# Kernel optimization log

Hardware: AMD Instinct MI355X
Metric: run time of the kernel (lower is better)

The kernel has to match this reference:

```python
import jax, jax.numpy as jnp
import numpy as np

B, L, H = 4096, 512, 32  # batch, latent_dim, hidden_size


def setup_inputs() -> dict:
    key = jax.random.key(0)
    ks = jax.random.split(key, 8)
    mu = jax.random.normal(ks[0], (B, L), jnp.float32)
    log_var = jax.random.normal(ks[1], (B, L), jnp.float32)
    eps0 = jax.random.normal(ks[2], (B,), jnp.float32)
    eps = jax.random.normal(ks[3], (B, L), jnp.float32)
    # Per-step MiniSampler params. Sampler idx has in_size = idx+1.
    # Zero-pad first-layer weights to [L, H, L]; row idx only uses cols 0..idx.
    mask = (jnp.arange(L)[None, :] <= jnp.arange(L)[:, None]).astype(jnp.float32)  # [L, L]
    W1 = jax.random.normal(ks[4], (L, H, L), jnp.float32) * 0.1 * mask[:, None, :]
    b1 = jax.random.normal(ks[5], (L, H), jnp.float32) * 0.1
    W2 = jax.random.normal(ks[6], (L, 2, H), jnp.float32) * 0.1
    b2 = jax.random.normal(ks[7], (L, 2), jnp.float32) * 0.1
    return {"mu": mu, "log_var": log_var, "eps0": eps0, "eps": eps,
            "W1": W1, "b1": b1, "W2": W2, "b2": b2}


def reference(mu, log_var, eps0, eps, W1, b1, W2, b2):
    # sample=False path (the default). First latent is reparameterized:
    std0 = jnp.exp(0.5 * log_var[:, 0])
    input0 = eps0 * std0 + mu[:, 0]                      # [B]
    # Input to sampler idx is [input0, mu[:,0], ..., mu[:,idx-1]];
    # W1 is column-masked so one shared padded vector works for all steps.
    v = jnp.concatenate([input0[:, None], mu[:, :-1]], axis=1)  # [B, L]
    h = jax.nn.leaky_relu(jnp.einsum('bj,ihj->bih', v, W1) + b1[None])  # [B, L, H]
    out = jnp.einsum('bih,ioh->bio', h, W2) + b2[None]   # [B, L, 2]
    mus_resampled = out[..., 0]                          # [B, L]
    log_vars_resampled = out[..., 1]                     # [B, L]
    samples = eps * jnp.exp(0.5 * log_vars_resampled) + mus_resampled  # [B, L]
    return (mus_resampled, log_vars_resampled, samples)
```

## Files before the change

### kernel.cpp

```cpp
#include <hip/hip_runtime.h>
#include <hip/hip_bf16.h>

#define Bn 4096
#define Ln 512
#define Hn 32
#define MT 4

using bf16x8 = __attribute__((ext_vector_type(8))) __bf16;
using f32x4  = __attribute__((ext_vector_type(4))) float;

#define GLOAD_LDS16(g, l)                                                          \
  __builtin_amdgcn_global_load_lds(                                                \
      (const __attribute__((address_space(1))) void*)(g),                          \
      (__attribute__((address_space(3))) void*)(l), 16, 0, 0)

__device__ __forceinline__ unsigned short f2bf(float x) {
  unsigned int u = __float_as_uint(x);
  unsigned int r = (u + 0x7FFFu + ((u >> 16) & 1u)) >> 16;
  return (unsigned short)r;
}

__global__ __launch_bounds__(256) void prep_w1_kernel(const float* __restrict__ W1,
                                                      unsigned short* __restrict__ W1b) {
  int idx = blockIdx.x * 256 + threadIdx.x;
  const float4 f = reinterpret_cast<const float4*>(W1)[idx];
  ushort4 o;
  o.x = f2bf(f.x); o.y = f2bf(f.y); o.z = f2bf(f.z); o.w = f2bf(f.w);
  reinterpret_cast<ushort4*>(W1b)[idx] = o;
}

__global__ __launch_bounds__(256) void prep_v_kernel(const float* __restrict__ mu,
                                                     const float* __restrict__ log_var,
                                                     const float* __restrict__ eps0,
                                                     unsigned short* __restrict__ Vb) {
  int idx = blockIdx.x * 256 + threadIdx.x;
  int b = idx >> 9, j = idx & 511;
  float v;
  if (j == 0) {
    v = eps0[b] * expf(0.5f * log_var[(size_t)b * Ln]) + mu[(size_t)b * Ln];
  } else {
    v = mu[(size_t)b * Ln + j - 1];
  }
  Vb[idx] = f2bf(v);
}

__global__ __launch_bounds__(256) void gemm_fused_kernel(
    const unsigned short* __restrict__ Vb,
    const unsigned short* __restrict__ W1b,
    const float* __restrict__ b1,
    const float* __restrict__ W2,
    const float* __restrict__ b2,
    const float* __restrict__ eps,
    float* __restrict__ out)
{
  const int tid  = threadIdx.x;
  const int wid  = tid >> 6;
  const int lane = tid & 63;
  const int l15  = lane & 15;
  const int lq   = lane >> 4;

  const int bid = blockIdx.x;
  const int bn  = 127 - (bid >> 3);
  const int mg  = bid & 7;
  const int mb  = mg * (MT * 128);
  const int nb  = bn * 128;

  const int ksteps = min(8, (bn + 16) >> 4);

  __shared__ unsigned short As[2 * 128 * 64];
  __shared__ unsigned short Bs[2 * 128 * 64];

  const int rowc = lane >> 3;
  const int sswz = (lane & 7) ^ rowc;
  const unsigned short* gA = Vb  + (size_t)(mb + wid * 32 + rowc) * Ln + sswz * 8;
  const unsigned short* gB = W1b + (size_t)(nb + wid * 32 + rowc) * Ln + sswz * 8;
  unsigned short* lA = As + wid * 2048;
  unsigned short* lB = Bs + wid * 2048;

  auto STAGE = [&](int buf, int mt, int k0e) {
    const int    lofs = buf * 8192;
    const size_t ga   = (size_t)mt * (128 * Ln) + k0e;
#pragma unroll
    for (int j = 0; j < 4; ++j) {
      GLOAD_LDS16(gA + ga + (size_t)j * 8 * Ln, lA + lofs + j * 512);
      GLOAD_LDS16(gB + k0e + (size_t)j * 8 * Ln, lB + lofs + j * 512);
    }
  };

  const int arow = (wid >> 1) * 64 + l15;
  const int brow = (wid & 1) * 64 + l15;
  const int swz7 = l15 & 7;

  f32x4 acc[4][4];
#pragma unroll
  for (int fn = 0; fn < 4; ++fn)
#pragma unroll
    for (int fm = 0; fm < 4; ++fm) acc[fn][fm] = f32x4{0.f, 0.f, 0.f, 0.f};

  auto COMPUTE = [&](int buf) {
    const int cofs = buf * 8192;
#pragma unroll
    for (int ks2 = 0; ks2 < 2; ++ks2) {
      const int se = ((ks2 * 4 + lq) ^ swz7) * 8;
      bf16x8 a[4], b[4];
#pragma unroll
      for (int f = 0; f < 4; ++f) {
        a[f] = *reinterpret_cast<const bf16x8*>(As + cofs + (arow + f * 16) * 64 + se);
        b[f] = *reinterpret_cast<const bf16x8*>(Bs + cofs + (brow + f * 16) * 64 + se);
      }
#pragma unroll
      for (int fn = 0; fn < 4; ++fn)
#pragma unroll
        for (int fm = 0; fm < 4; ++fm)
          acc[fn][fm] = __builtin_amdgcn_mfma_f32_16x16x32_bf16(b[fn], a[fm], acc[fn][fm], 0, 0, 0);
    }
  };

  float* mus = out;
  float* lvs = out + (size_t)Bn * Ln;
  float* smp = out + (size_t)2 * Bn * Ln;

  int buf = 0;
  STAGE(0, 0, 0);

  for (int mt = 0; mt < MT; ++mt) {
    for (int k = 0; k < ksteps; ++k) {
      int kn = k + 1, mtn = mt;
      if (kn == ksteps) { kn = 0; ++mtn; }
      if (mtn < MT) {
        STAGE(buf ^ 1, mtn, kn * 64);
        asm volatile("s_waitcnt vmcnt(8)" ::: "memory");
      } else {
        asm volatile("s_waitcnt vmcnt(0)" ::: "memory");
      }
      __builtin_amdgcn_s_barrier();
      __builtin_amdgcn_sched_barrier(0);
      COMPUTE(buf);

      if (k == ksteps - 1) {
        float* S = reinterpret_cast<float*>(Bs + buf * 8192);
        __builtin_amdgcn_s_barrier();

        const int wrow = (wid >> 1) * 64;
#pragma unroll
        for (int il = 0; il < 2; ++il) {
          const int i   = bn * 4 + (wid & 1) * 2 + il;
          const int icl = (wid & 1) * 2 + il;
          float4 b1q[2], w20q[2], w21q[2];
#pragma unroll
          for (int q = 0; q < 2; ++q) {
            const int hb = q * 16 + lq * 4;
            b1q[q]  = *reinterpret_cast<const float4*>(b1 + i * Hn + hb);
            w20q[q] = *reinterpret_cast<const float4*>(W2 + (i * 2 + 0) * Hn + hb);
            w21q[q] = *reinterpret_cast<const float4*>(W2 + (i * 2 + 1) * Hn + hb);
          }
          const float bias0 = b2[i * 2 + 0];
          const float bias1 = b2[i * 2 + 1];
#pragma unroll
          for (int fm = 0; fm < 4; ++fm) {
            float p0 = 0.f, p1 = 0.f;
#pragma unroll
            for (int q = 0; q < 2; ++q) {
              const f32x4& A = acc[il * 2 + q][fm];
              const float* b1f = reinterpret_cast<const float*>(&b1q[q]);
              const float* w0f = reinterpret_cast<const float*>(&w20q[q]);
              const float* w1f = reinterpret_cast<const float*>(&w21q[q]);
#pragma unroll
              for (int r = 0; r < 4; ++r) {
                float x  = A[r] + b1f[r];
                float hv = (x >= 0.f) ? x : 0.01f * x;
                p0 += hv * w0f[r];
                p1 += hv * w1f[r];
              }
            }
            p0 += __shfl_xor(p0, 16);
            p0 += __shfl_xor(p0, 32);
            p1 += __shfl_xor(p1, 16);
            p1 += __shfl_xor(p1, 32);
            if (lq == 0) {
              const int r = wrow + fm * 16 + l15;
              S[icl * 128 + r]       = p0 + bias0;
              S[512 + icl * 128 + r] = p1 + bias1;
            }
          }
        }
        asm volatile("s_waitcnt lgkmcnt(0)" ::: "memory");
        __builtin_amdgcn_s_barrier();

        if (tid < 128) {
          const int    r = tid;
          const size_t o = (size_t)(mb + mt * 128 + r) * Ln + bn * 4;
          float4 muv, lvv;
          muv.x = S[r];       muv.y = S[128 + r]; muv.z = S[256 + r]; muv.w = S[384 + r];
          lvv.x = S[512 + r]; lvv.y = S[640 + r]; lvv.z = S[768 + r]; lvv.w = S[896 + r];
          const float4 ep = *reinterpret_cast<const float4*>(eps + o);
          float4 sm;
          sm.x = ep.x * expf(0.5f * lvv.x) + muv.x;
          sm.y = ep.y * expf(0.5f * lvv.y) + muv.y;
          sm.z = ep.z * expf(0.5f * lvv.z) + muv.z;
          sm.w = ep.w * expf(0.5f * lvv.w) + muv.w;
          *reinterpret_cast<float4*>(mus + o) = muv;
          *reinterpret_cast<float4*>(lvs + o) = lvv;
          *reinterpret_cast<float4*>(smp + o) = sm;
        }
#pragma unroll
        for (int fn = 0; fn < 4; ++fn)
#pragma unroll
          for (int fm = 0; fm < 4; ++fm) acc[fn][fm] = f32x4{0.f, 0.f, 0.f, 0.f};
      }
      __builtin_amdgcn_s_barrier();
      buf ^= 1;
    }
  }
}

extern "C" void kernel_launch(void* const* d_in, const int* in_sizes, int n_in,
                              void* d_out, int out_size, void* d_ws, size_t ws_size,
                              hipStream_t stream) {
  const float* mu      = (const float*)d_in[0];
  const float* log_var = (const float*)d_in[1];
  const float* eps0    = (const float*)d_in[2];
  const float* eps     = (const float*)d_in[3];
  const float* W1      = (const float*)d_in[4];
  const float* b1      = (const float*)d_in[5];
  const float* W2      = (const float*)d_in[6];
  const float* b2      = (const float*)d_in[7];
  float* out = (float*)d_out;

  unsigned short* Vb  = (unsigned short*)d_ws;
  unsigned short* W1b = (unsigned short*)((char*)d_ws + (size_t)Bn * Ln * 2);

  prep_v_kernel<<<(Bn * Ln) / 256, 256, 0, stream>>>(mu, log_var, eps0, Vb);
  prep_w1_kernel<<<(Ln * Hn * Ln) / 4 / 256, 256, 0, stream>>>(W1, W1b);
  gemm_fused_kernel<<<128 * (32 / MT), 256, 0, stream>>>(
      Vb, W1b, b1, W2, b2, eps, out);
}
```

Measured before the change: 85.64 us.

## Load A operands directly to registers, skip masked W1 reads, remap blocks per XCD

The GEMM kernel no longer stages the V (A) tile through LDS. Each wave loads its A fragments straight from global memory into registers before the barrier, which halves LDS usage and allows an occupancy hint of 3 blocks per CU. Blocks are remapped so each XCD gets a balanced mix of triangular column tiles. The W1 conversion kernel skips reading the zero-masked upper triangle and writes zeros instead, and leaky_relu and exp are replaced with fmax and exp2. The risks are uncoalesced direct global loads of A and the changed vmcnt accounting.

Result: slower. 127.1 us (+48.4%).

```diff
diff --git a/kernel.cpp b/kernel.cpp
--- a/kernel.cpp
+++ b/kernel.cpp
@@ -23,9 +23,16 @@
 __global__ __launch_bounds__(256) void prep_w1_kernel(const float* __restrict__ W1,
                                                       unsigned short* __restrict__ W1b) {
   int idx = blockIdx.x * 256 + threadIdx.x;
-  const float4 f = reinterpret_cast<const float4*>(W1)[idx];
+  const int n  = idx >> 7;
+  const int c0 = (idx & 127) * 4;
+  const int i  = n >> 5;
   ushort4 o;
-  o.x = f2bf(f.x); o.y = f2bf(f.y); o.z = f2bf(f.z); o.w = f2bf(f.w);
+  if (c0 > i) {
+    o.x = 0; o.y = 0; o.z = 0; o.w = 0;
+  } else {
+    const float4 f = reinterpret_cast<const float4*>(W1)[idx];
+    o.x = f2bf(f.x); o.y = f2bf(f.y); o.z = f2bf(f.z); o.w = f2bf(f.w);
+  }
   reinterpret_cast<ushort4*>(W1b)[idx] = o;
 }
 
@@ -44,7 +51,7 @@
   Vb[idx] = f2bf(v);
 }
 
-__global__ __launch_bounds__(256) void gemm_fused_kernel(
+__global__ __launch_bounds__(256, 3) void gemm_fused_kernel(
     const unsigned short* __restrict__ Vb,
     const unsigned short* __restrict__ W1b,
     const float* __restrict__ b1,
@@ -59,35 +66,32 @@
   const int l15  = lane & 15;
   const int lq   = lane >> 4;
 
-  const int bid = blockIdx.x;
-  const int bn  = 127 - (bid >> 3);
-  const int mg  = bid & 7;
-  const int mb  = mg * (MT * 128);
-  const int nb  = bn * 128;
+  const int bid  = blockIdx.x;
+  const int xcd  = bid & 7;
+  const int s    = bid >> 3;
+  const int g    = xcd + 8 * (3 - (s >> 5));
+  const int bn   = g * 4 + ((s >> 3) & 3);
+  const int mg   = s & 7;
+  const int mb   = mg * (MT * 128);
+  const int nb   = bn * 128;
 
   const int ksteps = min(8, (bn + 16) >> 4);
 
-  __shared__ unsigned short As[2 * 128 * 64];
   __shared__ unsigned short Bs[2 * 128 * 64];
 
   const int rowc = lane >> 3;
   const int sswz = (lane & 7) ^ rowc;
-  const unsigned short* gA = Vb  + (size_t)(mb + wid * 32 + rowc) * Ln + sswz * 8;
   const unsigned short* gB = W1b + (size_t)(nb + wid * 32 + rowc) * Ln + sswz * 8;
-  unsigned short* lA = As + wid * 2048;
   unsigned short* lB = Bs + wid * 2048;
 
-  auto STAGE = [&](int buf, int mt, int k0e) {
-    const int    lofs = buf * 8192;
-    const size_t ga   = (size_t)mt * (128 * Ln) + k0e;
-#pragma unroll
-    for (int j = 0; j < 4; ++j) {
-      GLOAD_LDS16(gA + ga + (size_t)j * 8 * Ln, lA + lofs + j * 512);
-      GLOAD_LDS16(gB + k0e + (size_t)j * 8 * Ln, lB + lofs + j * 512);
-    }
+  auto STAGE_B = [&](int buf, int k0e) {
+#pragma unroll
+    for (int j = 0; j < 4; ++j)
+      GLOAD_LDS16(gB + k0e + (size_t)j * 8 * Ln, lB + buf * 8192 + j * 512);
   };
 
-  const int arow = (wid >> 1) * 64 + l15;
+  const unsigned short* gA = Vb + (size_t)(mb + (wid >> 1) * 64 + l15) * Ln;
+
   const int brow = (wid & 1) * 64 + l15;
   const int swz7 = l15 & 7;
 
@@ -96,46 +100,55 @@
   for (int fn = 0; fn < 4; ++fn)
 #pragma unroll
     for (int fm = 0; fm < 4; ++fm) acc[fn][fm] = f32x4{0.f, 0.f, 0.f, 0.f};
-
-  auto COMPUTE = [&](int buf) {
-    const int cofs = buf * 8192;
-#pragma unroll
-    for (int ks2 = 0; ks2 < 2; ++ks2) {
-      const int se = ((ks2 * 4 + lq) ^ swz7) * 8;
-      bf16x8 a[4], b[4];
-#pragma unroll
-      for (int f = 0; f < 4; ++f) {
-        a[f] = *reinterpret_cast<const bf16x8*>(As + cofs + (arow + f * 16) * 64 + se);
-        b[f] = *reinterpret_cast<const bf16x8*>(Bs + cofs + (brow + f * 16) * 64 + se);
-      }
-#pragma unroll
-      for (int fn = 0; fn < 4; ++fn)
-#pragma unroll
-        for (int fm = 0; fm < 4; ++fm)
-          acc[fn][fm] = __builtin_amdgcn_mfma_f32_16x16x32_bf16(b[fn], a[fm], acc[fn][fm], 0, 0, 0);
-    }
-  };
 
   float* mus = out;
   float* lvs = out + (size_t)Bn * Ln;
   float* smp = out + (size_t)2 * Bn * Ln;
 
   int buf = 0;
-  STAGE(0, 0, 0);
+  STAGE_B(0, 0);
 
   for (int mt = 0; mt < MT; ++mt) {
     for (int k = 0; k < ksteps; ++k) {
       int kn = k + 1, mtn = mt;
       if (kn == ksteps) { kn = 0; ++mtn; }
-      if (mtn < MT) {
-        STAGE(buf ^ 1, mtn, kn * 64);
+      const bool more = (mtn < MT);
+      if (more) STAGE_B(buf ^ 1, kn * 64);
+
+      bf16x8 a[2][4];
+      {
+        const unsigned short* pa = gA + (size_t)mt * (128 * Ln) + k * 64;
+#pragma unroll
+        for (int ks2 = 0; ks2 < 2; ++ks2)
+#pragma unroll
+          for (int f = 0; f < 4; ++f)
+            a[ks2][f] = *reinterpret_cast<const bf16x8*>(
+                pa + (size_t)f * 16 * Ln + (ks2 * 4 + lq) * 8);
+      }
+
+      if (more) {
+        asm volatile("s_waitcnt vmcnt(12)" ::: "memory");
+      } else {
         asm volatile("s_waitcnt vmcnt(8)" ::: "memory");
-      } else {
-        asm volatile("s_waitcnt vmcnt(0)" ::: "memory");
       }
       __builtin_amdgcn_s_barrier();
       __builtin_amdgcn_sched_barrier(0);
-      COMPUTE(buf);
+
+      const int cofs = buf * 8192;
+#pragma unroll
+      for (int ks2 = 0; ks2 < 2; ++ks2) {
+        const int se = ((ks2 * 4 + lq) ^ swz7) * 8;
+        bf16x8 b[4];
+#pragma unroll
+        for (int f = 0; f < 4; ++f)
+          b[f] = *reinterpret_cast<const bf16x8*>(Bs + cofs + (brow + f * 16) * 64 + se);
+#pragma unroll
+        for (int fn = 0; fn < 4; ++fn)
+#pragma unroll
+          for (int fm = 0; fm < 4; ++fm)
+            acc[fn][fm] = __builtin_amdgcn_mfma_f32_16x16x32_bf16(b[fn], a[ks2][fm],
+                                                                  acc[fn][fm], 0, 0, 0);
+      }
 
       if (k == ksteps - 1) {
         float* S = reinterpret_cast<float*>(Bs + buf * 8192);
@@ -168,7 +181,7 @@
 #pragma unroll
               for (int r = 0; r < 4; ++r) {
                 float x  = A[r] + b1f[r];
-                float hv = (x >= 0.f) ? x : 0.01f * x;
+                float hv = fmaxf(x, 0.01f * x);
                 p0 += hv * w0f[r];
                 p1 += hv * w1f[r];
               }
@@ -195,10 +208,10 @@
           lvv.x = S[512 + r]; lvv.y = S[640 + r]; lvv.z = S[768 + r]; lvv.w = S[896 + r];
           const float4 ep = *reinterpret_cast<const float4*>(eps + o);
           float4 sm;
-          sm.x = ep.x * expf(0.5f * lvv.x) + muv.x;
-          sm.y = ep.y * expf(0.5f * lvv.y) + muv.y;
-          sm.z = ep.z * expf(0.5f * lvv.z) + muv.z;
-          sm.w = ep.w * expf(0.5f * lvv.w) + muv.w;
+          sm.x = ep.x * __builtin_exp2f(lvv.x * 0.7213475204444817f) + muv.x;
+          sm.y = ep.y * __builtin_exp2f(lvv.y * 0.7213475204444817f) + muv.y;
+          sm.z = ep.z * __builtin_exp2f(lvv.z * 0.7213475204444817f) + muv.z;
+          sm.w = ep.w * __builtin_exp2f(lvv.w * 0.7213475204444817f) + muv.w;
           *reinterpret_cast<float4*>(mus + o) = muv;
           *reinterpret_cast<float4*>(lvs + o) = lvv;
           *reinterpret_cast<float4*>(smp + o) = sm;
```
